# Kernel optimization log

Hardware: AMD Instinct MI355X
Metric: run time of the kernel (lower is better)

## Reference

```python
import jax, jax.numpy as jnp
import numpy as np

B, S, I, H = 64, 1024, 256, 256  # batch, seq_len, input_size, hidden_size (2 layers)


def _gru_layer(x, W_ih, W_hh, b_ih, b_hh):
    """Run a torch.nn.GRUCell-equivalent layer over time. x: [B,S,in] -> [B,S,H]."""
    Hd = W_hh.shape[1]
    # Precompute input-side gate projections for all timesteps (math-equivalent).
    xg = jnp.einsum('bsi,gi->bsg', x, W_ih) + b_ih  # [B,S,3H]

    def step(h, xg_t):
        hg = h @ W_hh.T + b_hh                      # [B,3H]
        xr, xz, xn = jnp.split(xg_t, 3, axis=-1)
        hr, hz, hn = jnp.split(hg, 3, axis=-1)
        r = jax.nn.sigmoid(xr + hr)
        z = jax.nn.sigmoid(xz + hz)
        n = jnp.tanh(xn + r * hn)
        h_new = (1.0 - z) * n + z * h
        return h_new, h_new

    h0 = jnp.zeros((x.shape[0], Hd), dtype=x.dtype)
    _, hs = jax.lax.scan(step, h0, jnp.swapaxes(xg, 0, 1))  # scan over time
    return jnp.swapaxes(hs, 0, 1)  # [B,S,H]


def setup_inputs() -> dict:
    key = jax.random.key(0)
    ks = jax.random.split(key, 9)
    s_i = 1.0 / np.sqrt(H)
    u = lambda k, shape: jax.random.uniform(k, shape, jnp.float32, -s_i, s_i)
    return {
        'inputs': jax.random.normal(ks[0], (B, S, I), dtype=jnp.float32),
        'W_ih0': u(ks[1], (3 * H, I)),
        'W_hh0': u(ks[2], (3 * H, H)),
        'b_ih0': u(ks[3], (3 * H,)),
        'b_hh0': u(ks[4], (3 * H,)),
        'W_ih1': u(ks[5], (3 * H, H)),
        'W_hh1': u(ks[6], (3 * H, H)),
        'b_ih1': u(ks[7], (3 * H,)),
        'b_hh1': u(ks[8], (3 * H,)),
    }


def reference(inputs, W_ih0, W_hh0, b_ih0, b_hh0, W_ih1, W_hh1, b_ih1, b_hh1):
    h1 = _gru_layer(inputs, W_ih0, W_hh0, b_ih0, b_hh0)  # layer 0 states [B,S,H]
    h2 = _gru_layer(h1, W_ih1, W_hh1, b_ih1, b_hh1)      # layer 1 states [B,S,H]
    # return_sequences=True: (last-layer states, concat of all layers' states)
    return h2, jnp.concatenate([h1, h2], axis=2)
```

## Files before the change

kernel.cpp:

```cpp
#include <hip/hip_runtime.h>
#include <hip/hip_fp16.h>

#define BB 64
#define SS 1024
#define HD 256
#define GG 768

typedef _Float16 h2_t __attribute__((ext_vector_type(2)));
typedef _Float16 h8_t __attribute__((ext_vector_type(8)));

#define FDOT2(a, b, c) __builtin_amdgcn_fdot2((a), (b), (c), false)

__device__ __forceinline__ float sigm(float x) {
    return 1.0f / (1.0f + __expf(-x));
}
__device__ __forceinline__ float tanh_fast(float x) {
    float e = __expf(2.0f * fabsf(x));
    float t = 1.0f - 2.0f / (e + 1.0f);
    return copysignf(t, x);
}

__device__ __forceinline__ float quad_reduce(float x) {
    int t = __builtin_amdgcn_update_dpp(0, __float_as_int(x), 0xB1, 0xF, 0xF, true);
    x += __int_as_float(t);
    t = __builtin_amdgcn_update_dpp(0, __float_as_int(x), 0x4E, 0xF, 0xF, true);
    x += __int_as_float(t);
    return x;
}

__device__ __forceinline__ void load_wslices(const float* W, int wv, int row, int sl, h2_t w[4][32]) {
#pragma unroll
    for (int q = 0; q < 4; q++) {
        const float2* wr = (const float2*)(W + (size_t)(wv * 64 + row + 16 * q) * 256 + sl * 64);
#pragma unroll
        for (int k = 0; k < 32; k++) {
            float2 f = wr[k];
            h2_t p; p.x = (_Float16)f.x; p.y = (_Float16)f.y;
            w[q][k] = p;
        }
    }
}

__device__ __forceinline__ int swz256(int k) {
    int ksl = k >> 6;
    return ksl * 128 + ((((k >> 3) & 7) + 2 * ksl) & 7) * 16 + (k & 7) * 2;
}

__device__ __forceinline__ void dot_slices(const char* tbase, int sl, const h2_t w[4][32], float acc[4]) {
    const char* base = tbase + sl * 128;
#pragma unroll
    for (int j = 0; j < 8; j++) {
        h8_t v = *(const h8_t*)(base + ((((j + 2 * sl) & 7)) << 4));
        h2_t p0, p1, p2, p3;
        p0.x = v[0]; p0.y = v[1];
        p1.x = v[2]; p1.y = v[3];
        p2.x = v[4]; p2.y = v[5];
        p3.x = v[6]; p3.y = v[7];
#pragma unroll
        for (int q = 0; q < 4; q++) {
            acc[q] = FDOT2(w[q][4 * j + 0], p0, acc[q]);
            acc[q] = FDOT2(w[q][4 * j + 1], p1, acc[q]);
            acc[q] = FDOT2(w[q][4 * j + 2], p2, acc[q]);
            acc[q] = FDOT2(w[q][4 * j + 3], p3, acc[q]);
        }
    }
}

__device__ __forceinline__ void wait_ge(unsigned* f, unsigned v) {
    if (threadIdx.x == 0) {
        while (__hip_atomic_load(f, __ATOMIC_RELAXED, __HIP_MEMORY_SCOPE_AGENT) < v)
            __builtin_amdgcn_s_sleep(2);
        (void)__hip_atomic_load(f, __ATOMIC_ACQUIRE, __HIP_MEMORY_SCOPE_AGENT);
    }
    __syncthreads();
}
__device__ __forceinline__ void publish(unsigned* f, unsigned v) {
    __syncthreads();
    if (threadIdx.x == 0)
        __hip_atomic_store(f, v, __ATOMIC_RELEASE, __HIP_MEMORY_SCOPE_AGENT);
}

__global__ __launch_bounds__(GG, 3) void gru_pipe(
    const float* __restrict__ X,
    const float* __restrict__ Wih0, const float* __restrict__ bih0,
    const float* __restrict__ Whh0, const float* __restrict__ bhh0,
    const float* __restrict__ Wih1, const float* __restrict__ bih1,
    const float* __restrict__ Whh1, const float* __restrict__ bhh1,
    float* __restrict__ h2out, float* __restrict__ cat,
    float* __restrict__ ring0, float* __restrict__ ring1,
    unsigned* __restrict__ prog, int CT, int NS, int NC)
{
    __shared__ h8_t xs[2048];
    __shared__ float hf[HD], rs[HD], zs[HD];

    const int role = blockIdx.x >> 6;
    const int b    = blockIdx.x & 63;
    const int g    = threadIdx.x;
    const int wv   = g >> 6;
    const int l    = g & 63;
    const int row  = l >> 2;
    const int sl   = l & 3;
    const int out  = wv * 64 + row + 16 * sl;

    unsigned* f_p0 = prog + (0 * 64 + b) * 16;
    unsigned* f_p1 = prog + (1 * 64 + b) * 16;
    unsigned* f_r0 = prog + (2 * 64 + b) * 16;
    unsigned* f_r1 = prog + (3 * 64 + b) * 16;

    h2_t w[4][32];

    if (role == 0 || role == 1) {
        const float* Wp   = (role == 0) ? Wih0 : Wih1;
        const float* bp   = (role == 0) ? bih0 : bih1;
        const float* Xs   = (role == 0) ? X : cat;
        const int xstride = (role == 0) ? 256 : 512;
        float* ringo      = (role == 0) ? ring0 : ring1;
        unsigned* f_up    = (role == 0) ? nullptr : f_r0;
        unsigned* f_cons  = (role == 0) ? f_r0 : f_r1;
        unsigned* f_out   = (role == 0) ? f_p0 : f_p1;

        load_wslices(Wp, wv, row, sl, w);
        const float bv = bp[out];
        char* xb = (char*)xs;

        for (int c = 0; c < NC; c++) {
            if (f_up) wait_ge(f_up, c + 1);
            if (c >= NS) wait_ge(f_cons, c - NS + 1);
            const int t0 = c * CT;
            for (int idx = g; idx < CT * 256; idx += GG) {
                int tt = idx >> 8, k = idx & 255;
                *(_Float16*)(xb + tt * 512 + swz256(k)) =
                    (_Float16)Xs[((size_t)b * SS + t0 + tt) * xstride + k];
            }
            __syncthreads();
            float* ro = ringo + ((size_t)b * NS + (c % NS)) * ((size_t)CT * GG) + out;
            for (int tt = 0; tt < CT; tt++) {
                float acc[4] = {0.f, 0.f, 0.f, 0.f};
                dot_slices(xb + tt * 512, sl, w, acc);
                float g0 = quad_reduce(acc[0]);
                float g1 = quad_reduce(acc[1]);
                float g2 = quad_reduce(acc[2]);
                float g3 = quad_reduce(acc[3]);
                float mine = (sl == 0) ? g0 : (sl == 1) ? g1 : (sl == 2) ? g2 : g3;
                ro[(size_t)tt * GG] = mine + bv;
            }
            publish(f_out, c + 1);
        }
    } else {
        const float* Wp    = (role == 2) ? Whh0 : Whh1;
        const float* bp    = (role == 2) ? bhh0 : bhh1;
        const float* ringi = (role == 2) ? ring0 : ring1;
        unsigned* f_in  = (role == 2) ? f_p0 : f_p1;
        unsigned* f_out = (role == 2) ? f_r0 : f_r1;
        float* outA   = (role == 2) ? cat : h2out;
        int   strideA = (role == 2) ? 512 : 256;
        float* outB   = (role == 2) ? nullptr : (cat + 256);

        load_wslices(Wp, wv, row, sl, w);
        const float bv = bp[out];
        const int cls = wv >> 2;
        const int i   = out & 255;
        char* xb = (char*)xs;
        _Float16* hws = (_Float16*)(xb + swz256(i));

        if (g < HD) { hf[g] = 0.0f; ((unsigned short*)xs)[g] = 0; }
        __syncthreads();

        for (int c = 0; c < NC; c++) {
            wait_ge(f_in, c + 1);
            const float* xgp = ringi + ((size_t)b * NS + (c % NS)) * ((size_t)CT * GG) + out;
            float xv = xgp[0];
            for (int tt = 0; tt < CT; tt++) {
                float xv_next = (tt + 1 < CT) ? xgp[(size_t)(tt + 1) * GG] : 0.0f;
                float acc[4] = {0.f, 0.f, 0.f, 0.f};
                dot_slices(xb, sl, w, acc);
                float g0 = quad_reduce(acc[0]);
                float g1 = quad_reduce(acc[1]);
                float g2 = quad_reduce(acc[2]);
                float g3 = quad_reduce(acc[3]);
                float hd = ((sl == 0) ? g0 : (sl == 1) ? g1 : (sl == 2) ? g2 : g3) + bv;
                if (cls == 0)      rs[i] = sigm(xv + hd);
                else if (cls == 1) zs[i] = sigm(xv + hd);
                __syncthreads();
                if (cls == 2) {
                    float r = rs[i], z = zs[i], hp = hf[i];
                    float n = tanh_fast(xv + r * hd);
                    float hnew = (1.0f - z) * n + z * hp;
                    hf[i] = hnew;
                    *hws = (_Float16)hnew;
                    size_t t = (size_t)(c * CT + tt);
                    outA[((size_t)b * SS + t) * strideA + i] = hnew;
                    if (outB) outB[((size_t)b * SS + t) * 512 + i] = hnew;
                }
                __syncthreads();
                xv = xv_next;
            }
            publish(f_out, c + 1);
        }
    }
}

extern "C" void kernel_launch(void* const* d_in, const int* in_sizes, int n_in,
                              void* d_out, int out_size, void* d_ws, size_t ws_size,
                              hipStream_t stream)
{
    const float* inputs = (const float*)d_in[0];
    const float* W_ih0  = (const float*)d_in[1];
    const float* W_hh0  = (const float*)d_in[2];
    const float* b_ih0  = (const float*)d_in[3];
    const float* b_hh0  = (const float*)d_in[4];
    const float* W_ih1  = (const float*)d_in[5];
    const float* W_hh1  = (const float*)d_in[6];
    const float* b_ih1  = (const float*)d_in[7];
    const float* b_hh1  = (const float*)d_in[8];

    float* h2out = (float*)d_out;
    float* cat   = h2out + (size_t)BB * SS * HD;

    unsigned char* ws = (unsigned char*)d_ws;
    unsigned* prog = (unsigned*)ws;
    const size_t FLAG_BYTES = 4 * 64 * 16 * sizeof(unsigned);
    size_t avail = ws_size > FLAG_BYTES ? ws_size - FLAG_BYTES : 0;

    int CT = 64, NS = 0;
    for (;;) {
        size_t slot = (size_t)BB * CT * GG * sizeof(float);
        size_t m = slot ? avail / (2 * slot) : 0;
        int nc = SS / CT;
        NS = (int)(m < (size_t)nc ? m : (size_t)nc);
        if (NS >= 2 || CT == 8) break;
        CT >>= 1;
    }
    if (NS < 1) NS = 1;
    int NC = SS / CT;

    float* ring0 = (float*)(ws + FLAG_BYTES);
    float* ring1 = ring0 + (size_t)BB * NS * CT * GG;

    hipMemsetAsync(prog, 0, FLAG_BYTES, stream);
    gru_pipe<<<256, GG, 0, stream>>>(inputs,
                                     W_ih0, b_ih0, W_hh0, b_hh0,
                                     W_ih1, b_ih1, W_hh1, b_hh1,
                                     h2out, cat, ring0, ring1, prog, CT, NS, NC);
}
```

Measured before the change: 1.812 ms.

## Compute all three GRU gates per thread with 256-thread blocks

Each block now uses 256 threads instead of 768, and each thread holds the weight slices for all three gates (r, z, n) of one hidden unit. The recurrent step can then apply the gate nonlinearities and the state update in registers. This removes the shared-memory exchange of r and z and one barrier per timestep. The hidden state is double-buffered in LDS so a single barrier per step is enough. The cost is triple the register footprint per thread (384 packed-half weight registers) with only one wave per SIMD, which risks spills and leaves little latency hiding for the serial dot products.

Measured after the change: 2.289 ms. 1.26x slower.

```diff
diff --git a/kernel.cpp b/kernel.cpp
--- a/kernel.cpp
+++ b/kernel.cpp
@@ -5,6 +5,7 @@
 #define SS 1024
 #define HD 256
 #define GG 768
+#define NT 256
 
 typedef _Float16 h2_t __attribute__((ext_vector_type(2)));
 typedef _Float16 h8_t __attribute__((ext_vector_type(8)));
@@ -28,42 +29,52 @@
     return x;
 }
 
-__device__ __forceinline__ void load_wslices(const float* W, int wv, int row, int sl, h2_t w[4][32]) {
-#pragma unroll
-    for (int q = 0; q < 4; q++) {
-        const float2* wr = (const float2*)(W + (size_t)(wv * 64 + row + 16 * q) * 256 + sl * 64);
-#pragma unroll
-        for (int k = 0; k < 32; k++) {
-            float2 f = wr[k];
-            h2_t p; p.x = (_Float16)f.x; p.y = (_Float16)f.y;
-            w[q][k] = p;
-        }
-    }
-}
-
 __device__ __forceinline__ int swz256(int k) {
     int ksl = k >> 6;
     return ksl * 128 + ((((k >> 3) & 7) + 2 * ksl) & 7) * 16 + (k & 7) * 2;
 }
 
-__device__ __forceinline__ void dot_slices(const char* tbase, int sl, const h2_t w[4][32], float acc[4]) {
+__device__ __forceinline__ void load_w3(const float* W, int wv, int r_, int sl, h2_t w[3][4][32]) {
+#pragma unroll
+    for (int gi = 0; gi < 3; gi++) {
+#pragma unroll
+        for (int q = 0; q < 4; q++) {
+            const float2* wr = (const float2*)(W + (size_t)(gi * 256 + wv * 64 + r_ + 16 * q) * 256 + sl * 64);
+#pragma unroll
+            for (int k = 0; k < 32; k++) {
+                float2 f = wr[k];
+                h2_t p; p.x = (_Float16)f.x; p.y = (_Float16)f.y;
+                w[gi][q][k] = p;
+            }
+        }
+    }
+}
+
+__device__ __forceinline__ void dot12(const char* tbase, int sl, const h2_t w[3][4][32], float acc[3][4]) {
     const char* base = tbase + sl * 128;
 #pragma unroll
     for (int j = 0; j < 8; j++) {
-        h8_t v = *(const h8_t*)(base + ((((j + 2 * sl) & 7)) << 4));
+        h8_t v = *(const h8_t*)(base + (((j + 2 * sl) & 7) << 4));
         h2_t p0, p1, p2, p3;
         p0.x = v[0]; p0.y = v[1];
         p1.x = v[2]; p1.y = v[3];
         p2.x = v[4]; p2.y = v[5];
         p3.x = v[6]; p3.y = v[7];
 #pragma unroll
-        for (int q = 0; q < 4; q++) {
-            acc[q] = FDOT2(w[q][4 * j + 0], p0, acc[q]);
-            acc[q] = FDOT2(w[q][4 * j + 1], p1, acc[q]);
-            acc[q] = FDOT2(w[q][4 * j + 2], p2, acc[q]);
-            acc[q] = FDOT2(w[q][4 * j + 3], p3, acc[q]);
-        }
-    }
+        for (int gi = 0; gi < 3; gi++) {
+#pragma unroll
+            for (int q = 0; q < 4; q++) {
+                acc[gi][q] = FDOT2(w[gi][q][4 * j + 0], p0, acc[gi][q]);
+                acc[gi][q] = FDOT2(w[gi][q][4 * j + 1], p1, acc[gi][q]);
+                acc[gi][q] = FDOT2(w[gi][q][4 * j + 2], p2, acc[gi][q]);
+                acc[gi][q] = FDOT2(w[gi][q][4 * j + 3], p3, acc[gi][q]);
+            }
+        }
+    }
+}
+
+__device__ __forceinline__ float pick4(const float a[4], int sl) {
+    return sl == 0 ? a[0] : sl == 1 ? a[1] : sl == 2 ? a[2] : a[3];
 }
 
 __device__ __forceinline__ void wait_ge(unsigned* f, unsigned v) {
@@ -80,7 +91,7 @@
         __hip_atomic_store(f, v, __ATOMIC_RELEASE, __HIP_MEMORY_SCOPE_AGENT);
 }
 
-__global__ __launch_bounds__(GG, 3) void gru_pipe(
+__global__ __launch_bounds__(NT, 1) void gru_pipe(
     const float* __restrict__ X,
     const float* __restrict__ Wih0, const float* __restrict__ bih0,
     const float* __restrict__ Whh0, const float* __restrict__ bhh0,
@@ -91,23 +102,22 @@
     unsigned* __restrict__ prog, int CT, int NS, int NC)
 {
     __shared__ h8_t xs[2048];
-    __shared__ float hf[HD], rs[HD], zs[HD];
 
     const int role = blockIdx.x >> 6;
     const int b    = blockIdx.x & 63;
     const int g    = threadIdx.x;
     const int wv   = g >> 6;
     const int l    = g & 63;
-    const int row  = l >> 2;
+    const int r_   = l >> 2;
     const int sl   = l & 3;
-    const int out  = wv * 64 + row + 16 * sl;
+    const int i    = wv * 64 + r_ + 16 * sl;
 
     unsigned* f_p0 = prog + (0 * 64 + b) * 16;
     unsigned* f_p1 = prog + (1 * 64 + b) * 16;
     unsigned* f_r0 = prog + (2 * 64 + b) * 16;
     unsigned* f_r1 = prog + (3 * 64 + b) * 16;
 
-    h2_t w[4][32];
+    h2_t w[3][4][32];
 
     if (role == 0 || role == 1) {
         const float* Wp   = (role == 0) ? Wih0 : Wih1;
@@ -119,30 +129,37 @@
         unsigned* f_cons  = (role == 0) ? f_r0 : f_r1;
         unsigned* f_out   = (role == 0) ? f_p0 : f_p1;
 
-        load_wslices(Wp, wv, row, sl, w);
-        const float bv = bp[out];
+        load_w3(Wp, wv, r_, sl, w);
+        const float b0 = bp[i], b1 = bp[256 + i], b2 = bp[512 + i];
         char* xb = (char*)xs;
 
         for (int c = 0; c < NC; c++) {
             if (f_up) wait_ge(f_up, c + 1);
             if (c >= NS) wait_ge(f_cons, c - NS + 1);
             const int t0 = c * CT;
-            for (int idx = g; idx < CT * 256; idx += GG) {
+            for (int idx = g; idx < CT * 256; idx += NT) {
                 int tt = idx >> 8, k = idx & 255;
                 *(_Float16*)(xb + tt * 512 + swz256(k)) =
                     (_Float16)Xs[((size_t)b * SS + t0 + tt) * xstride + k];
             }
             __syncthreads();
-            float* ro = ringo + ((size_t)b * NS + (c % NS)) * ((size_t)CT * GG) + out;
+            float* ro = ringo + ((size_t)b * NS + (c % NS)) * ((size_t)CT * GG);
             for (int tt = 0; tt < CT; tt++) {
-                float acc[4] = {0.f, 0.f, 0.f, 0.f};
-                dot_slices(xb + tt * 512, sl, w, acc);
-                float g0 = quad_reduce(acc[0]);
-                float g1 = quad_reduce(acc[1]);
-                float g2 = quad_reduce(acc[2]);
-                float g3 = quad_reduce(acc[3]);
-                float mine = (sl == 0) ? g0 : (sl == 1) ? g1 : (sl == 2) ? g2 : g3;
-                ro[(size_t)tt * GG] = mine + bv;
+                float acc[3][4] = {};
+                dot12(xb + tt * 512, sl, w, acc);
+                float ar = quad_reduce(acc[0][0]), a1 = quad_reduce(acc[0][1]),
+                      a2 = quad_reduce(acc[0][2]), a3 = quad_reduce(acc[0][3]);
+                float zr = quad_reduce(acc[1][0]), z1 = quad_reduce(acc[1][1]),
+                      z2 = quad_reduce(acc[1][2]), z3 = quad_reduce(acc[1][3]);
+                float nr = quad_reduce(acc[2][0]), n1 = quad_reduce(acc[2][1]),
+                      n2 = quad_reduce(acc[2][2]), n3 = quad_reduce(acc[2][3]);
+                float fa[4] = {ar, a1, a2, a3};
+                float fz[4] = {zr, z1, z2, z3};
+                float fn[4] = {nr, n1, n2, n3};
+                float* rt = ro + (size_t)tt * GG;
+                rt[i]       = pick4(fa, sl) + b0;
+                rt[256 + i] = pick4(fz, sl) + b1;
+                rt[512 + i] = pick4(fn, sl) + b2;
             }
             publish(f_out, c + 1);
         }
@@ -156,44 +173,52 @@
         int   strideA = (role == 2) ? 512 : 256;
         float* outB   = (role == 2) ? nullptr : (cat + 256);
 
-        load_wslices(Wp, wv, row, sl, w);
-        const float bv = bp[out];
-        const int cls = wv >> 2;
-        const int i   = out & 255;
+        load_w3(Wp, wv, r_, sl, w);
+        const float b0 = bp[i], b1 = bp[256 + i], b2 = bp[512 + i];
         char* xb = (char*)xs;
-        _Float16* hws = (_Float16*)(xb + swz256(i));
-
-        if (g < HD) { hf[g] = 0.0f; ((unsigned short*)xs)[g] = 0; }
+        _Float16* hws0 = (_Float16*)(xb + swz256(i));
+        _Float16* hws1 = (_Float16*)(xb + 512 + swz256(i));
+        float hprev = 0.0f;
+
+        ((unsigned short*)xs)[g] = 0;
         __syncthreads();
 
         for (int c = 0; c < NC; c++) {
             wait_ge(f_in, c + 1);
-            const float* xgp = ringi + ((size_t)b * NS + (c % NS)) * ((size_t)CT * GG) + out;
-            float xv = xgp[0];
+            const float* xgp = ringi + ((size_t)b * NS + (c % NS)) * ((size_t)CT * GG);
+            float xr = xgp[i], xz = xgp[256 + i], xn = xgp[512 + i];
             for (int tt = 0; tt < CT; tt++) {
-                float xv_next = (tt + 1 < CT) ? xgp[(size_t)(tt + 1) * GG] : 0.0f;
-                float acc[4] = {0.f, 0.f, 0.f, 0.f};
-                dot_slices(xb, sl, w, acc);
-                float g0 = quad_reduce(acc[0]);
-                float g1 = quad_reduce(acc[1]);
-                float g2 = quad_reduce(acc[2]);
-                float g3 = quad_reduce(acc[3]);
-                float hd = ((sl == 0) ? g0 : (sl == 1) ? g1 : (sl == 2) ? g2 : g3) + bv;
-                if (cls == 0)      rs[i] = sigm(xv + hd);
-                else if (cls == 1) zs[i] = sigm(xv + hd);
+                float xr2 = 0.f, xz2 = 0.f, xn2 = 0.f;
+                if (tt + 1 < CT) {
+                    const float* nx = xgp + (size_t)(tt + 1) * GG;
+                    xr2 = nx[i]; xz2 = nx[256 + i]; xn2 = nx[512 + i];
+                }
+                float acc[3][4] = {};
+                dot12(xb + ((tt & 1) << 9), sl, w, acc);
+                float a0 = quad_reduce(acc[0][0]), a1 = quad_reduce(acc[0][1]),
+                      a2 = quad_reduce(acc[0][2]), a3 = quad_reduce(acc[0][3]);
+                float c0 = quad_reduce(acc[1][0]), c1 = quad_reduce(acc[1][1]),
+                      c2 = quad_reduce(acc[1][2]), c3 = quad_reduce(acc[1][3]);
+                float d0 = quad_reduce(acc[2][0]), d1 = quad_reduce(acc[2][1]),
+                      d2 = quad_reduce(acc[2][2]), d3 = quad_reduce(acc[2][3]);
+                float fa[4] = {a0, a1, a2, a3};
+                float fc[4] = {c0, c1, c2, c3};
+                float fd[4] = {d0, d1, d2, d3};
+                float hr = pick4(fa, sl) + b0;
+                float hz = pick4(fc, sl) + b1;
+                float hn = pick4(fd, sl) + b2;
+                float rg = sigm(xr + hr);
+                float zg = sigm(xz + hz);
+                float ng = tanh_fast(xn + rg * hn);
+                float hnew = (1.0f - zg) * ng + zg * hprev;
+                hprev = hnew;
+                _Float16* hw = (tt & 1) ? hws0 : hws1;
+                *hw = (_Float16)hnew;
+                size_t t = (size_t)(c * CT + tt);
+                outA[((size_t)b * SS + t) * strideA + i] = hnew;
+                if (outB) outB[((size_t)b * SS + t) * 512 + i] = hnew;
                 __syncthreads();
-                if (cls == 2) {
-                    float r = rs[i], z = zs[i], hp = hf[i];
-                    float n = tanh_fast(xv + r * hd);
-                    float hnew = (1.0f - z) * n + z * hp;
-                    hf[i] = hnew;
-                    *hws = (_Float16)hnew;
-                    size_t t = (size_t)(c * CT + tt);
-                    outA[((size_t)b * SS + t) * strideA + i] = hnew;
-                    if (outB) outB[((size_t)b * SS + t) * 512 + i] = hnew;
-                }
-                __syncthreads();
-                xv = xv_next;
+                xr = xr2; xz = xz2; xn = xn2;
             }
             publish(f_out, c + 1);
         }
@@ -238,7 +263,7 @@
     float* ring1 = ring0 + (size_t)BB * NS * CT * GG;
 
     hipMemsetAsync(prog, 0, FLAG_BYTES, stream);
-    gru_pipe<<<256, GG, 0, stream>>>(inputs,
+    gru_pipe<<<256, NT, 0, stream>>>(inputs,
                                      W_ih0, b_ih0, W_hh0, b_hh0,
                                      W_ih1, b_ih1, W_hh1, b_hh1,
                                      h2out, cat, ring0, ring1, prog, CT, NS, NC);
```
